# Kernel optimization log

Hardware: AMD Instinct MI355X
Metric: run time of the kernel (lower is better)

The kernel has to match this reference:

```python
import jax, jax.numpy as jnp
import numpy as np

L = 3          # GRU layers
H = 512        # hidden_dim == latent_dim == atom_vocab_size (required for source to run)
V = 512        # atom_vocab_size
B = 16
S = 96


def setup_inputs() -> dict:
    key = jax.random.key(0)
    ks = jax.random.split(key, 16)
    p = lambda k, shape: jax.random.normal(k, shape, dtype=jnp.float32) * 0.05
    return {
        "z": jax.random.normal(ks[0], (B, H), dtype=jnp.float32),
        "W_l2h": p(ks[1], (H, H)), "b_l2h": p(ks[2], (H,)),
        # GRU weights, torch gate order (r, z, n); stored [in, 3H] so x @ W
        "W_ih": p(ks[3], (L, H, 3 * H)), "W_hh": p(ks[4], (L, H, 3 * H)),
        "b_ih": p(ks[5], (L, 3 * H)), "b_hh": p(ks[6], (L, 3 * H)),
        # atom predictor MLP
        "Wa1": p(ks[7], (H, H)), "ba1": p(ks[8], (H,)),
        "Wa2": p(ks[9], (H, V)), "ba2": p(ks[10], (V,)),
        # bond predictor MLP (in = 2*V = 2*H)
        "Wb1": p(ks[11], (2 * H, H)), "bb1": p(ks[12], (H,)),
        "Wb2": p(ks[13], (H, 4)), "bb2": p(ks[14], (4,)),
        "target_length": S,
    }


def _gru_cell(hl, x, Wih_l, Whh_l, bih_l, bhh_l):
    gi = x @ Wih_l + bih_l          # [B, 3H]
    gh = hl @ Whh_l + bhh_l         # [B, 3H]
    ir, iz, inn = jnp.split(gi, 3, axis=-1)
    hr, hz, hn = jnp.split(gh, 3, axis=-1)
    r = jax.nn.sigmoid(ir + hr)
    zg = jax.nn.sigmoid(iz + hz)
    n = jnp.tanh(inn + r * hn)
    return (1.0 - zg) * n + zg * hl


def reference(z, W_l2h, b_l2h, W_ih, W_hh, b_ih, b_hh,
              Wa1, ba1, Wa2, ba2, Wb1, bb1, Wb2, bb2, target_length):
    batch = z.shape[0]
    seq_len = target_length
    h0 = z @ W_l2h + b_l2h                         # [B, H]
    hidden0 = jnp.broadcast_to(h0[None], (L, batch, H))  # repeat over layers

    x0 = jnp.zeros((batch, H), dtype=z.dtype)      # decoder input is zeros each step

    def step(hs, _):
        x = x0
        new = []
        for l in range(L):
            hl = _gru_cell(hs[l], x, W_ih[l], W_hh[l], b_ih[l], b_hh[l])
            new.append(hl)
            x = hl                                  # no inter-layer dropout (eval)
        logits = jax.nn.relu(x @ Wa1 + ba1) @ Wa2 + ba2   # [B, V]
        return jnp.stack(new), logits

    _, atoms = jax.lax.scan(step, hidden0, None, length=seq_len)  # [S, B, V]
    atoms = atoms.transpose(1, 0, 2)                # [B, S, V]
    atom_indices = jnp.argmax(atoms, axis=-1)       # argmax(softmax) == argmax(logits)

    # all-pairs bond MLP, vectorized: split first linear to avoid [B,S,S,2V] concat
    e_i = atoms @ Wb1[:V]                           # [B, S, H] (contribution of atom i)
    e_j = atoms @ Wb1[V:]                           # [B, S, H] (contribution of atom j)
    hp = jax.nn.relu(e_i[:, :, None, :] + e_j[:, None, :, :] + bb1)  # [B, S, S, H]
    edge = hp @ Wb2 + bb2                           # [B, S, S, 4]
    mask = 1.0 - jnp.eye(seq_len, dtype=edge.dtype)  # i == j entries stay zero
    edge = edge * mask[None, :, :, None]
    return atom_indices, edge
```

## Files before the change

### kernel.cpp

```cpp
#include <hip/hip_runtime.h>
#include <math.h>

#define H    512
#define TH3  1536
#define GRID 224

#define WS_STATE(l,p) ((size_t)((l)*3+(p)) * 8192)
#define WS_A1(p)      ((size_t)73728 + (size_t)(p)*8192)
#define WS_ATOMS      ((size_t)98304)
#define WS_E          ((size_t)884736)

__device__ __forceinline__ float sigm_(float x) { return 1.0f / (1.0f + expf(-x)); }

__device__ __forceinline__ float stampf(float x, unsigned b) {
    return __uint_as_float((__float_as_uint(x) & ~1u) | b);
}
__device__ __forceinline__ int lsb4ok(float4 v, unsigned e) {
    return ((__float_as_uint(v.x) & 1u) == e) & ((__float_as_uint(v.y) & 1u) == e) &
           ((__float_as_uint(v.z) & 1u) == e) & ((__float_as_uint(v.w) & 1u) == e);
}

__device__ __forceinline__ void ld_coh4(const float* p0, const float* p1,
                                        const float* p2, const float* p3,
                                        float4& a, float4& b, float4& c, float4& d)
{
    asm volatile(
        "global_load_dwordx4 %0, %4, off sc0 sc1\n\t"
        "global_load_dwordx4 %1, %5, off sc0 sc1\n\t"
        "global_load_dwordx4 %2, %6, off sc0 sc1\n\t"
        "global_load_dwordx4 %3, %7, off sc0 sc1\n\t"
        "s_waitcnt vmcnt(0)"
        : "=&v"(a), "=&v"(b), "=&v"(c), "=&v"(d)
        : "v"(p0), "v"(p1), "v"(p2), "v"(p3)
        : "memory");
}

__device__ __forceinline__ void ld_coh8(const float* p0, const float* p1,
                                        const float* p2, const float* p3,
                                        const float* p4, const float* p5,
                                        const float* p6, const float* p7,
                                        float4& a, float4& b, float4& c, float4& d,
                                        float4& e, float4& f, float4& g, float4& h)
{
    asm volatile(
        "global_load_dwordx4 %0, %8, off sc0 sc1\n\t"
        "global_load_dwordx4 %1, %9, off sc0 sc1\n\t"
        "global_load_dwordx4 %2, %10, off sc0 sc1\n\t"
        "global_load_dwordx4 %3, %11, off sc0 sc1\n\t"
        "global_load_dwordx4 %4, %12, off sc0 sc1\n\t"
        "global_load_dwordx4 %5, %13, off sc0 sc1\n\t"
        "global_load_dwordx4 %6, %14, off sc0 sc1\n\t"
        "global_load_dwordx4 %7, %15, off sc0 sc1\n\t"
        "s_waitcnt vmcnt(0)"
        : "=&v"(a), "=&v"(b), "=&v"(c), "=&v"(d),
          "=&v"(e), "=&v"(f), "=&v"(g), "=&v"(h)
        : "v"(p0), "v"(p1), "v"(p2), "v"(p3),
          "v"(p4), "v"(p5), "v"(p6), "v"(p7)
        : "memory");
}

__device__ __forceinline__ void st_coh1(float* p, float v) {
    asm volatile("global_store_dword %0, %1, off sc0 sc1" :: "v"(p), "v"(v) : "memory");
}

__device__ __forceinline__ void ld_coh_u32x2(const unsigned* p0, const unsigned* p1,
                                             unsigned& a, unsigned& b)
{
    asm volatile(
        "global_load_dword %0, %2, off sc0 sc1\n\t"
        "global_load_dword %1, %3, off sc0 sc1\n\t"
        "s_waitcnt vmcnt(0)"
        : "=&v"(a), "=&v"(b)
        : "v"(p0), "v"(p1)
        : "memory");
}

__device__ __forceinline__ void st_coh_u32(unsigned* p, unsigned v) {
    asm volatile("global_store_dword %0, %1, off sc0 sc1" :: "v"(p), "v"(v) : "memory");
}

template<int CTRL>
__device__ __forceinline__ float dppmov(float v) {
    return __int_as_float(__builtin_amdgcn_update_dpp(
        0, __float_as_int(v), CTRL, 0xF, 0xF, true));
}
#define DPP_XOR1 0xB1
#define DPP_XOR2 0x4E
#define DPP_XOR8 0x128

template<int PAT>
__device__ __forceinline__ float swzf(float v) {
    return __int_as_float(__builtin_amdgcn_ds_swizzle(__float_as_int(v), PAT));
}
#define SWZ_XOR4  0x101F
#define SWZ_XOR16 0x401F

extern "C" __global__ __launch_bounds__(256)
void k_init(const float* __restrict__ z, const float* __restrict__ Wl2h,
            const float* __restrict__ bl2h, float* __restrict__ ws)
{
    if (blockIdx.x == 0)
        ((unsigned*)(ws + WS_E))[threadIdx.x] = 0u;
    const int t  = threadIdx.x;
    const int jl = t & 15, b = t >> 4;
    const int j  = blockIdx.x * 16 + jl;
    float acc = 0.f;
    #pragma unroll 4
    for (int k = 0; k < H; ++k)
        acc += z[b * H + k] * Wl2h[(size_t)k * H + j];
    acc += bl2h[j];

    const int preh[3][3] = { { 1, 0, -1 },
                             { 0, -1, 1 },
                             { -1, 1, 0 } };
    #pragma unroll
    for (int l = 0; l < 3; ++l)
        #pragma unroll
        for (int p = 0; p < 3; ++p) {
            float v = (preh[l][p] < 0) ? stampf(acc, 1u)
                                       : __uint_as_float((unsigned)preh[l][p]);
            ws[WS_STATE(l, p) + j * 16 + b] = v;
        }
    const unsigned preA1[3] = { 1u, 0u, 0u };
    #pragma unroll
    for (int p = 0; p < 3; ++p)
        ws[WS_A1(p) + j * 16 + b] = __uint_as_float(preA1[p]);
}

__global__ __launch_bounds__(512, 2)
void k_gru(const float* __restrict__ W_ih, const float* __restrict__ W_hh,
           const float* __restrict__ b_ih, const float* __restrict__ b_hh,
           const float* __restrict__ Wa1,  const float* __restrict__ ba1,
           const float* __restrict__ Wa2,  const float* __restrict__ ba2,
           float* __restrict__ ws)
{
    __shared__ float sx[10240];
    __shared__ float sx2[10240];
    __shared__ float sh[10240];
    __shared__ float red[1536];
    unsigned* flags = (unsigned*)(ws + WS_E);

    const int bid = blockIdx.x;
    const int tid = threadIdx.x;

    int job, jbase;
    if      (bid < 64)  { job = 0; jbase = bid * 8; }
    else if (bid < 128) { job = 1; jbase = (bid - 64) * 8; }
    else if (bid < 192) { job = 2; jbase = (bid - 128) * 8; }
    else if (bid < 208) { job = 3; jbase = (bid - 192) * 32; }
    else                { job = 4; jbase = (bid - 208) * 32; }

    const int ks = tid & 31;
    const int cs = tid >> 6;

    int rs0, rc0;
    if      (job == 0) { rs0 = 0;   rc0 = 128; }
    else if (job == 1) { rs0 = 64;  rc0 = 128; }
    else if (job == 2) { rs0 = 128; rc0 = 80;  }
    else if (job == 3) { rs0 = 208; rc0 = 16;  }
    else               { rs0 = 0;   rc0 = 0;   }
    int fidl[2];
    #pragma unroll
    for (int e = 0; e < 2; ++e) {
        int idx = (tid & 63) + e * 64;
        fidl[e] = (idx < rc0) ? rs0 + idx : bid;
    }

    float w[6][16];
    if (job <= 2) {
        const int khalf = cs & 1, cpair = cs >> 1;
        const int colbase = jbase + cpair * 2;
        const float* WB = W_hh + (size_t)job * H * TH3;
        const float* WA = W_ih + (size_t)job * H * TH3;
        #pragma unroll
        for (int f = 0; f < 6; ++f) {
            int g = f >> 1, c = f & 1;
            #pragma unroll
            for (int kk = 0; kk < 8; ++kk) {
                size_t ro = (size_t)(khalf * 256 + kk * 32 + ks) * TH3 + g * 512 + colbase + c;
                w[f][8 + kk] = WB[ro];
                if (job != 0) w[f][kk] = WA[ro];
            }
        }
    } else {
        const float* base = (job == 3) ? Wa1 : Wa2;
        const int colbase = jbase + cs * 4;
        #pragma unroll
        for (int f = 0; f < 4; ++f)
            #pragma unroll
            for (int kk = 0; kk < 16; ++kk)
                w[f][kk] = base[(size_t)(kk * 32 + ks) * H + colbase + f];
    }

    float c_bi0 = 0, c_bi1 = 0, c_bi2 = 0, c_bh0 = 0, c_bh1 = 0, c_bh2 = 0;
    float hp = 0.f, c_ba = 0.f;
    if (job <= 2) {
        if (tid < 128) {
            int b = tid & 15, j2 = tid >> 4, jc = jbase + j2;
            const float* bi  = b_ih + (size_t)job * TH3;
            const float* bhh = b_hh + (size_t)job * TH3;
            c_bi0 = bi[jc]; c_bi1 = bi[512 + jc]; c_bi2 = bi[1024 + jc];
            c_bh0 = bhh[jc]; c_bh1 = bhh[512 + jc]; c_bh2 = bhh[1024 + jc];
            const int hpp = (job == 0) ? 2 : (job == 1) ? 1 : 0;
            hp = ws[WS_STATE(job, hpp) + jc * 16 + b];
        }
    } else if (job == 3) {
        c_ba = ba1[jbase + (tid >> 4)];
    } else {
        c_ba = ba2[jbase + (tid & 31)];
    }

    auto stage32k = [&](const float* src, unsigned eb, float* dst) {
        const int k0 = tid >> 2, q4 = (tid & 3) * 4;
        float4 a, b, c, d;
        for (;;) {
            ld_coh4(src + 4 * tid, src + 4 * (tid + 512),
                    src + 4 * (tid + 1024), src + 4 * (tid + 1536), a, b, c, d);
            if (__all(lsb4ok(a, eb) & lsb4ok(b, eb) & lsb4ok(c, eb) & lsb4ok(d, eb)))
                break;
            __builtin_amdgcn_s_sleep(1);
        }
        *(float4*)&dst[(k0      ) * 20 + q4] = a;
        *(float4*)&dst[(k0 + 128) * 20 + q4] = b;
        *(float4*)&dst[(k0 + 256) * 20 + q4] = c;
        *(float4*)&dst[(k0 + 384) * 20 + q4] = d;
    };

    auto stage64k = [&](const float* srcH, const float* srcX, unsigned eb,
                        float* dstH, float* dstX) {
        const int k0 = tid >> 2, q4 = (tid & 3) * 4;
        float4 xa, xb, xc, xd, ha, hb, hc, hd;
        for (;;) {
            ld_coh8(srcX + 4 * tid, srcX + 4 * (tid + 512),
                    srcX + 4 * (tid + 1024), srcX + 4 * (tid + 1536),
                    srcH + 4 * tid, srcH + 4 * (tid + 512),
                    srcH + 4 * (tid + 1024), srcH + 4 * (tid + 1536),
                    xa, xb, xc, xd, ha, hb, hc, hd);
            int ok = lsb4ok(xa, eb) & lsb4ok(xb, eb) & lsb4ok(xc, eb) & lsb4ok(xd, eb) &
                     lsb4ok(ha, eb) & lsb4ok(hb, eb) & lsb4ok(hc, eb) & lsb4ok(hd, eb);
            if (__all(ok)) break;
            __builtin_amdgcn_s_sleep(1);
        }
        *(float4*)&dstX[(k0      ) * 20 + q4] = xa;
        *(float4*)&dstX[(k0 + 128) * 20 + q4] = xb;
        *(float4*)&dstX[(k0 + 256) * 20 + q4] = xc;
        *(float4*)&dstX[(k0 + 384) * 20 + q4] = xd;
        *(float4*)&dstH[(k0      ) * 20 + q4] = ha;
        *(float4*)&dstH[(k0 + 128) * 20 + q4] = hb;
        *(float4*)&dstH[(k0 + 256) * 20 + q4] = hc;
        *(float4*)&dstH[(k0 + 384) * 20 + q4] = hd;
    };

    auto mv6 = [&](const float* arr, int wo, int redbase) {
        const int qh = (tid >> 5) & 1;
        const int rowoff = 8 * qh;
        const bool b0 = (ks & 1), b1 = (ks & 2), b3 = (ks & 8), b4 = (ks & 16);
        const float* base = arr + (cs & 1) * (256 * 20);
        float acc[6][8];
        #pragma unroll
        for (int f = 0; f < 6; ++f)
            #pragma unroll
            for (int i = 0; i < 8; ++i) acc[f][i] = 0.f;
        #pragma unroll
        for (int kk = 0; kk < 8; ++kk) {
            const float* p = base + (kk * 32 + ks) * 20 + rowoff;
            float4 v0 = *(const float4*)p;
            float4 v1 = *(const float4*)(p + 4);
            #pragma unroll
            for (int f = 0; f < 6; ++f) {
                float wv = w[f][wo + kk];
                acc[f][0] += wv * v0.x; acc[f][1] += wv * v0.y;
                acc[f][2] += wv * v0.z; acc[f][3] += wv * v0.w;
                acc[f][4] += wv * v1.x; acc[f][5] += wv * v1.y;
                acc[f][6] += wv * v1.z; acc[f][7] += wv * v1.w;
            }
        }
        float a[6];
        #pragma unroll
        for (int f = 0; f < 6; ++f) {
            float t[4];
            #pragma unroll
            for (int j = 0; j < 4; ++j) {
                float give = b0 ? acc[f][j] : acc[f][j + 4];
                float recv = dppmov<DPP_XOR1>(give);
                float keep = b0 ? acc[f][j + 4] : acc[f][j];
                t[j] = keep + recv;
            }
            float u[2];
            #pragma unroll
            for (int j = 0; j < 2; ++j) {
                float give = b1 ? t[j] : t[j + 2];
                float recv = dppmov<DPP_XOR2>(give);
                float keep = b1 ? t[j + 2] : t[j];
                u[j] = keep + recv;
            }
            float give = b3 ? u[0] : u[1];
            float recv = dppmov<DPP_XOR8>(give);
            float keep = b3 ? u[1] : u[0];
            a[f] = keep + recv;
        }
        #pragma unroll
        for (int f = 0; f < 6; ++f) a[f] += swzf<SWZ_XOR4>(a[f]);
        float r[3];
        #pragma unroll
        for (int i = 0; i < 3; ++i) {
            float give = b4 ? a[i] : a[i + 3];
            float recv = swzf<SWZ_XOR16>(give);
            float keep = b4 ? a[i + 3] : a[i];
            r[i] = keep + recv;
        }
        if (!(ks & 4)) {
            int bl = ((ks & 1) << 2) | (ks & 2) | ((ks >> 3) & 1);
            int bb = ((tid >> 5) & 1) * 8 + bl;
            int fb3 = ((ks >> 4) & 1) * 3;
            #pragma unroll
            for (int i = 0; i < 3; ++i) {
                int f = fb3 + i, g = f >> 1, c = f & 1;
                red[redbase + (cs & 1) * 384 + g * 128 + ((cs >> 1) * 2 + c) * 16 + bb] = r[i];
            }
        }
    };

    auto mv4 = [&](const float* arr) {
        const int qh = (tid >> 5) & 1;
        const int rowoff = 8 * qh;
        const bool b0 = (ks & 1), b1 = (ks & 2), b3 = (ks & 8), b4 = (ks & 16);
        float acc[4][8];
        #pragma unroll
        for (int f = 0; f < 4; ++f)
            #pragma unroll
            for (int i = 0; i < 8; ++i) acc[f][i] = 0.f;
        #pragma unroll
        for (int kk = 0; kk < 16; ++kk) {
            const float* p = arr + (kk * 32 + ks) * 20 + rowoff;
            float4 v0 = *(const float4*)p;
            float4 v1 = *(const float4*)(p + 4);
            #pragma unroll
            for (int f = 0; f < 4; ++f) {
                float wv = w[f][kk];
                acc[f][0] += wv * v0.x; acc[f][1] += wv * v0.y;
                acc[f][2] += wv * v0.z; acc[f][3] += wv * v0.w;
                acc[f][4] += wv * v1.x; acc[f][5] += wv * v1.y;
                acc[f][6] += wv * v1.z; acc[f][7] += wv * v1.w;
            }
        }
        float a[4];
        #pragma unroll
        for (int f = 0; f < 4; ++f) {
            float t[4];
            #pragma unroll
            for (int j = 0; j < 4; ++j) {
                float give = b0 ? acc[f][j] : acc[f][j + 4];
                float recv = dppmov<DPP_XOR1>(give);
                float keep = b0 ? acc[f][j + 4] : acc[f][j];
                t[j] = keep + recv;
            }
            float u[2];
            #pragma unroll
            for (int j = 0; j < 2; ++j) {
                float give = b1 ? t[j] : t[j + 2];
                float recv = dppmov<DPP_XOR2>(give);
                float keep = b1 ? t[j + 2] : t[j];
                u[j] = keep + recv;
            }
            float give = b3 ? u[0] : u[1];
            float recv = dppmov<DPP_XOR8>(give);
            float keep = b3 ? u[1] : u[0];
            a[f] = keep + recv;
        }
        #pragma unroll
        for (int f = 0; f < 4; ++f) a[f] += swzf<SWZ_XOR4>(a[f]);
        float r[2];
        #pragma unroll
        for (int i = 0; i < 2; ++i) {
            float give = b4 ? a[i] : a[i + 2];
            float recv = swzf<SWZ_XOR16>(give);
            float keep = b4 ? a[i + 2] : a[i];
            r[i] = keep + recv;
        }
        if (!(ks & 4)) {
            int bl = ((ks & 1) << 2) | (ks & 2) | ((ks >> 3) & 1);
            int bb = ((tid >> 5) & 1) * 8 + bl;
            int f2 = ((ks >> 4) & 1) * 2;
            #pragma unroll
            for (int i = 0; i < 2; ++i)
                red[(cs * 4 + f2 + i) * 16 + bb] = r[i];
        }
    };

    for (int s = 0; s < 102; ++s) {
        const int rp = (s + 2) % 3, wp = s % 3;
        const unsigned expb = (unsigned)((s + 1) & 1);
        const unsigned myb  = (unsigned)(s & 1);
        int act;
        if      (job == 0) act = (s <= 95);
        else if (job == 1) act = (s >= 2 && s <= 97);
        else if (job == 2) act = (s >= 4 && s <= 99);
        else if (job == 3) act = (s >= 5 && s <= 100);
        else               act = (s >= 6 && s <= 101);
        const int s0 = (job == 1) ? 2 : 4;
        const int dox = (job == 1 || job == 2) && (s >= s0 - 1) && (s <= s0 + 94);
        float* rbuf = (s & 1) ? sx2 : sx;
        float* wbuf = (s & 1) ? sx : sx2;

        if (act) {
            if (tid < 64 && s >= 2) {
                unsigned lim = (unsigned)(s - 1);
                for (;;) {
                    unsigned v0, v1;
                    ld_coh_u32x2(&flags[fidl[0]], &flags[fidl[1]], v0, v1);
                    if (__all((int)((v0 >= lim) & (v1 >= lim)))) break;
                    __builtin_amdgcn_s_sleep(1);
                }
            }

            if (job == 1 || job == 2) {
                mv6(rbuf, 0, 0);
                if (dox)
                    stage64k(ws + WS_STATE(job, rp), ws + WS_STATE(job - 1, rp),
                             expb, sh, wbuf);
                else
                    stage32k(ws + WS_STATE(job, rp), expb, sh);
                __syncthreads();
                mv6(sh, 8, 768);
                __syncthreads();
                if (tid < 128) {
                    int b = tid & 15, jc = jbase + (tid >> 4);
                    int o = tid;
                    float gi0 = red[o]        + red[384 + o];
                    float gi1 = red[128 + o]  + red[512 + o];
                    float gi2 = red[256 + o]  + red[640 + o];
                    float gh0 = red[768 + o]  + red[1152 + o];
                    float gh1 = red[896 + o]  + red[1280 + o];
                    float gh2 = red[1024 + o] + red[1408 + o];
                    float r  = sigm_(gi0 + c_bi0 + gh0 + c_bh0);
                    float zg = sigm_(gi1 + c_bi1 + gh1 + c_bh1);
                    float n  = tanhf(gi2 + c_bi2 + r * (gh2 + c_bh2));
                    float hn = (1.f - zg) * n + zg * hp;
                    hp = hn;
                    st_coh1(&ws[WS_STATE(job, wp) + jc * 16 + b], stampf(hn, myb));
                }
            } else if (job == 0) {
                stage32k(ws + WS_STATE(0, rp), expb, sx);
                __syncthreads();
                mv6(sx, 8, 768);
                __syncthreads();
                if (tid < 128) {
                    int b = tid & 15, jc = jbase + (tid >> 4);
                    int o = tid;
                    float g0 = red[768 + o]  + red[1152 + o];
                    float g1 = red[896 + o]  + red[1280 + o];
                    float g2 = red[1024 + o] + red[1408 + o];
                    float r  = sigm_(c_bi0 + g0 + c_bh0);
                    float zg = sigm_(c_bi1 + g1 + c_bh1);
                    float n  = tanhf(c_bi2 + r * (g2 + c_bh2));
                    float hn = (1.f - zg) * n + zg * hp;
                    hp = hn;
                    st_coh1(&ws[WS_STATE(0, wp) + jc * 16 + b], stampf(hn, myb));
                }
            } else {
                const float* srcp = (job == 3) ? (ws + WS_STATE(2, rp))
                                               : (ws + WS_A1(rp));
                stage32k(srcp, expb, sx);
                __syncthreads();
                mv4(sx);
                __syncthreads();
                if (job == 3) {
                    int b = tid & 15, j2 = tid >> 4, jc = jbase + j2;
                    float v = red[j2 * 16 + b] + c_ba;
                    st_coh1(&ws[WS_A1(wp) + jc * 16 + b], stampf(fmaxf(v, 0.f), myb));
                } else {
                    int j2 = tid & 31, b = tid >> 5, jc = jbase + j2;
                    float v = red[j2 * 16 + b] + c_ba;
                    ws[WS_ATOMS + ((size_t)(s - 6) * 16 + b) * H + jc] = v;
                }
            }
        } else if (dox) {
            stage32k(ws + WS_STATE(job - 1, rp), expb, wbuf);
        }

        __syncthreads();
        if (tid == 0) st_coh_u32(&flags[bid], (unsigned)(s + 1));
    }
}

extern "C" __global__ __launch_bounds__(256)
void k_argmax(const float* __restrict__ ws, float* __restrict__ out)
{
    const int t = blockIdx.x;
    const int wv = threadIdx.x >> 6, lane = threadIdx.x & 63;
    for (int b = wv; b < 16; b += 4) {
        const float* row = ws + WS_ATOMS + ((size_t)t * 16 + b) * H;
        float mx = -3.4028235e38f; int mi = 0;
        #pragma unroll
        for (int c = 0; c < 8; ++c) {
            int idx = lane + c * 64;
            float v = row[idx];
            if (v > mx) { mx = v; mi = idx; }
        }
        #pragma unroll
        for (int off = 32; off >= 1; off >>= 1) {
            float omx = __shfl_down(mx, off);
            int   omi = __shfl_down(mi, off);
            if (omx > mx || (omx == mx && omi < mi)) { mx = omx; mi = omi; }
        }
        if (lane == 0) out[b * 96 + t] = (float)mi;
    }
}

extern "C" __global__ __launch_bounds__(256)
void k_eij(const float* __restrict__ Wb1, const float* __restrict__ bb1,
           float* __restrict__ ws)
{
    __shared__ float aT[8192];
    const int bid = blockIdx.x;
    const int t = bid >> 4, m = (bid >> 3) & 1, ct = bid & 7;
    const int tid = threadIdx.x;
    const float* atoms = ws + WS_ATOMS;
    for (int f = tid; f < 2048; f += 256) {
        int b = f >> 7, kq = f & 127;
        float4 v = ((const float4*)(atoms + ((size_t)(t * 16 + b)) * H))[kq];
        aT[(kq * 4 + 0) * 16 + b] = v.x;
        aT[(kq * 4 + 1) * 16 + b] = v.y;
        aT[(kq * 4 + 2) * 16 + b] = v.z;
        aT[(kq * 4 + 3) * 16 + b] = v.w;
    }
    __syncthreads();
    const int c = tid & 63, rq = tid >> 6;
    const int col = ct * 64 + c;
    const float* Wp = Wb1 + (size_t)m * H * H + col;
    float a0 = 0, a1 = 0, a2 = 0, a3 = 0;
    #pragma unroll 8
    for (int k = 0; k < 512; ++k) {
        float  wv = Wp[(size_t)k * H];
        float4 av = *(const float4*)&aT[k * 16 + rq * 4];
        a0 += av.x * wv; a1 += av.y * wv; a2 += av.z * wv; a3 += av.w * wv;
    }
    float bb = (m == 0) ? bb1[col] : 0.f;
    a0 += bb; a1 += bb; a2 += bb; a3 += bb;
    float* eb = ws + WS_E + (size_t)(m * 16) * 96 * H;
    eb[((size_t)(rq * 4 + 0) * 96 + t) * H + col] = a0;
    eb[((size_t)(rq * 4 + 1) * 96 + t) * H + col] = a1;
    eb[((size_t)(rq * 4 + 2) * 96 + t) * H + col] = a2;
    eb[((size_t)(rq * 4 + 3) * 96 + t) * H + col] = a3;
}

extern "C" __global__ __launch_bounds__(256)
void k_edge(const float* __restrict__ Wb2, const float* __restrict__ bb2,
            const float* __restrict__ ws, float* __restrict__ out)
{
    __shared__ float ls[32][260];
    __shared__ float wsm[2048];
    const int bid = blockIdx.x;
    const int b = bid / 36, r6 = bid % 36, it = r6 / 6, jt = r6 % 6;
    const int tid = threadIdx.x;
    const int ip = tid & 15, jp = tid >> 4;
    float acc0 = 0, acc1 = 0, acc2 = 0, acc3 = 0;

    for (int f = tid; f < 2048; f += 256)
        wsm[f] = Wb2[f];

    for (int ph = 0; ph < 2; ++ph) {
        __syncthreads();
        for (int f = tid; f < 2048; f += 256) {
            int r = f >> 6, c4 = f & 63;
            const float* src = (r < 16)
                ? ws + WS_E + ((size_t)b * 96 + it * 16 + r) * H
                : ws + WS_E + ((size_t)(16 + b) * 96 + jt * 16 + (r - 16)) * H;
            float4 v = *(const float4*)(src + ph * 256 + c4 * 4);
            *(float4*)&ls[r][c4 * 4] = v;
        }
        __syncthreads();
        const float* wb = &wsm[ph * 1024];
        #pragma unroll 2
        for (int hh = 0; hh < 256; hh += 4) {
            float4 ei = *(const float4*)&ls[ip][hh];
            float4 ej = *(const float4*)&ls[16 + jp][hh];
            float4 w0 = *(const float4*)(wb + (size_t)hh * 4);
            float4 w1 = *(const float4*)(wb + (size_t)hh * 4 + 4);
            float4 w2 = *(const float4*)(wb + (size_t)hh * 4 + 8);
            float4 w3 = *(const float4*)(wb + (size_t)hh * 4 + 12);
            float v;
            v = fmaxf(ei.x + ej.x, 0.f); acc0 += v * w0.x; acc1 += v * w0.y; acc2 += v * w0.z; acc3 += v * w0.w;
            v = fmaxf(ei.y + ej.y, 0.f); acc0 += v * w1.x; acc1 += v * w1.y; acc2 += v * w1.z; acc3 += v * w1.w;
            v = fmaxf(ei.z + ej.z, 0.f); acc0 += v * w2.x; acc1 += v * w2.y; acc2 += v * w2.z; acc3 += v * w2.w;
            v = fmaxf(ei.w + ej.w, 0.f); acc0 += v * w3.x; acc1 += v * w3.y; acc2 += v * w3.z; acc3 += v * w3.w;
        }
    }
    const int i = it * 16 + ip, j = jt * 16 + jp;
    float4 o;
    if (i == j) { o.x = 0.f; o.y = 0.f; o.z = 0.f; o.w = 0.f; }
    else { o.x = acc0 + bb2[0]; o.y = acc1 + bb2[1]; o.z = acc2 + bb2[2]; o.w = acc3 + bb2[3]; }
    *(float4*)(out + 1536 + (((size_t)b * 96 + i) * 96 + j) * 4) = o;
}

extern "C" void kernel_launch(void* const* d_in, const int* in_sizes, int n_in,
                              void* d_out, int out_size, void* d_ws, size_t ws_size,
                              hipStream_t stream)
{
    const float* z    = (const float*)d_in[0];
    const float* Wl2h = (const float*)d_in[1];
    const float* bl2h = (const float*)d_in[2];
    const float* W_ih = (const float*)d_in[3];
    const float* W_hh = (const float*)d_in[4];
    const float* b_ih = (const float*)d_in[5];
    const float* b_hh = (const float*)d_in[6];
    const float* Wa1  = (const float*)d_in[7];
    const float* ba1  = (const float*)d_in[8];
    const float* Wa2  = (const float*)d_in[9];
    const float* ba2  = (const float*)d_in[10];
    const float* Wb1  = (const float*)d_in[11];
    const float* bb1  = (const float*)d_in[12];
    const float* Wb2  = (const float*)d_in[13];
    const float* bb2  = (const float*)d_in[14];
    float* out = (float*)d_out;
    float* ws  = (float*)d_ws;

    hipLaunchKernelGGL(k_init, dim3(32), dim3(256), 0, stream, z, Wl2h, bl2h, ws);

    hipLaunchKernelGGL(k_gru, dim3(GRID), dim3(512), 0, stream,
                       W_ih, W_hh, b_ih, b_hh, Wa1, ba1, Wa2, ba2, ws);

    hipLaunchKernelGGL(k_argmax, dim3(96), dim3(256), 0, stream, ws, out);
    hipLaunchKernelGGL(k_eij, dim3(1536), dim3(256), 0, stream, Wb1, bb1, ws);
    hipLaunchKernelGGL(k_edge, dim3(576), dim3(256), 0, stream, Wb2, bb2, ws, out);
}
```

Measured before the change: 798.8 us.

## Post step flags early and prefetch GRU state loads before flag wait

Each block now publishes its step-completion flag right after staging its input into shared memory instead of at the end of the step, so producer blocks can overwrite the triple-buffered state sooner. For layers 1 and 2, the coherent loads of the input and hidden state are issued before the flag spin and the first matvec, and are waited on afterwards, hiding load latency behind compute. This relies on the triple buffering and LSB stamp checks to stay correct once flags are released early, and the prefetched values may be stale, which forces a reload loop.

```diff
diff --git a/kernel.cpp b/kernel.cpp
--- a/kernel.cpp
+++ b/kernel.cpp
@@ -59,6 +59,34 @@
         : "memory");
 }
 
+__device__ __forceinline__ void ld_coh8_issue(const float* p0, const float* p1,
+                                              const float* p2, const float* p3,
+                                              const float* p4, const float* p5,
+                                              const float* p6, const float* p7,
+                                              float4& a, float4& b, float4& c, float4& d,
+                                              float4& e, float4& f, float4& g, float4& h)
+{
+    asm volatile(
+        "global_load_dwordx4 %0, %8, off sc0 sc1\n\t"
+        "global_load_dwordx4 %1, %9, off sc0 sc1\n\t"
+        "global_load_dwordx4 %2, %10, off sc0 sc1\n\t"
+        "global_load_dwordx4 %3, %11, off sc0 sc1\n\t"
+        "global_load_dwordx4 %4, %12, off sc0 sc1\n\t"
+        "global_load_dwordx4 %5, %13, off sc0 sc1\n\t"
+        "global_load_dwordx4 %6, %14, off sc0 sc1\n\t"
+        "global_load_dwordx4 %7, %15, off sc0 sc1"
+        : "=&v"(a), "=&v"(b), "=&v"(c), "=&v"(d),
+          "=&v"(e), "=&v"(f), "=&v"(g), "=&v"(h)
+        : "v"(p0), "v"(p1), "v"(p2), "v"(p3),
+          "v"(p4), "v"(p5), "v"(p6), "v"(p7)
+        : "memory");
+}
+
+__device__ __forceinline__ void vm_wait0() {
+    asm volatile("s_waitcnt vmcnt(0)" ::: "memory");
+    __builtin_amdgcn_sched_barrier(0);
+}
+
 __device__ __forceinline__ void st_coh1(float* p, float v) {
     asm volatile("global_store_dword %0, %1, off sc0 sc1" :: "v"(p), "v"(v) : "memory");
 }
@@ -224,31 +252,6 @@
         *(float4*)&dst[(k0 + 128) * 20 + q4] = b;
         *(float4*)&dst[(k0 + 256) * 20 + q4] = c;
         *(float4*)&dst[(k0 + 384) * 20 + q4] = d;
-    };
-
-    auto stage64k = [&](const float* srcH, const float* srcX, unsigned eb,
-                        float* dstH, float* dstX) {
-        const int k0 = tid >> 2, q4 = (tid & 3) * 4;
-        float4 xa, xb, xc, xd, ha, hb, hc, hd;
-        for (;;) {
-            ld_coh8(srcX + 4 * tid, srcX + 4 * (tid + 512),
-                    srcX + 4 * (tid + 1024), srcX + 4 * (tid + 1536),
-                    srcH + 4 * tid, srcH + 4 * (tid + 512),
-                    srcH + 4 * (tid + 1024), srcH + 4 * (tid + 1536),
-                    xa, xb, xc, xd, ha, hb, hc, hd);
-            int ok = lsb4ok(xa, eb) & lsb4ok(xb, eb) & lsb4ok(xc, eb) & lsb4ok(xd, eb) &
-                     lsb4ok(ha, eb) & lsb4ok(hb, eb) & lsb4ok(hc, eb) & lsb4ok(hd, eb);
-            if (__all(ok)) break;
-            __builtin_amdgcn_s_sleep(1);
-        }
-        *(float4*)&dstX[(k0      ) * 20 + q4] = xa;
-        *(float4*)&dstX[(k0 + 128) * 20 + q4] = xb;
-        *(float4*)&dstX[(k0 + 256) * 20 + q4] = xc;
-        *(float4*)&dstX[(k0 + 384) * 20 + q4] = xd;
-        *(float4*)&dstH[(k0      ) * 20 + q4] = ha;
-        *(float4*)&dstH[(k0 + 128) * 20 + q4] = hb;
-        *(float4*)&dstH[(k0 + 256) * 20 + q4] = hc;
-        *(float4*)&dstH[(k0 + 384) * 20 + q4] = hd;
     };
 
     auto mv6 = [&](const float* arr, int wo, int redbase) {
@@ -402,26 +405,65 @@
         const int dox = (job == 1 || job == 2) && (s >= s0 - 1) && (s <= s0 + 94);
         float* rbuf = (s & 1) ? sx2 : sx;
         float* wbuf = (s & 1) ? sx : sx2;
+        bool posted = false;
 
         if (act) {
-            if (tid < 64 && s >= 2) {
-                unsigned lim = (unsigned)(s - 1);
-                for (;;) {
-                    unsigned v0, v1;
-                    ld_coh_u32x2(&flags[fidl[0]], &flags[fidl[1]], v0, v1);
-                    if (__all((int)((v0 >= lim) & (v1 >= lim)))) break;
-                    __builtin_amdgcn_s_sleep(1);
+            if (job == 1 || job == 2) {
+                const float* srcH = ws + WS_STATE(job, rp);
+                const float* srcX = ws + WS_STATE(job - 1, rp);
+                const int k0 = tid >> 2, q4 = (tid & 3) * 4;
+                float4 xa, xb, xc, xd, ha, hb, hc, hd;
+                if (dox)
+                    ld_coh8_issue(srcX + 4 * tid, srcX + 4 * (tid + 512),
+                                  srcX + 4 * (tid + 1024), srcX + 4 * (tid + 1536),
+                                  srcH + 4 * tid, srcH + 4 * (tid + 512),
+                                  srcH + 4 * (tid + 1024), srcH + 4 * (tid + 1536),
+                                  xa, xb, xc, xd, ha, hb, hc, hd);
+
+                if (tid < 64 && s >= 2) {
+                    unsigned lim = (unsigned)(s - 1);
+                    for (;;) {
+                        unsigned v0, v1;
+                        ld_coh_u32x2(&flags[fidl[0]], &flags[fidl[1]], v0, v1);
+                        if (__all((int)((v0 >= lim) & (v1 >= lim)))) break;
+                        __builtin_amdgcn_s_sleep(1);
+                    }
                 }
-            }
-
-            if (job == 1 || job == 2) {
+
                 mv6(rbuf, 0, 0);
-                if (dox)
-                    stage64k(ws + WS_STATE(job, rp), ws + WS_STATE(job - 1, rp),
-                             expb, sh, wbuf);
-                else
-                    stage32k(ws + WS_STATE(job, rp), expb, sh);
+
+                if (dox) {
+                    vm_wait0();
+                    int ok = lsb4ok(xa, expb) & lsb4ok(xb, expb) &
+                             lsb4ok(xc, expb) & lsb4ok(xd, expb) &
+                             lsb4ok(ha, expb) & lsb4ok(hb, expb) &
+                             lsb4ok(hc, expb) & lsb4ok(hd, expb);
+                    while (!__all(ok)) {
+                        __builtin_amdgcn_s_sleep(1);
+                        ld_coh8(srcX + 4 * tid, srcX + 4 * (tid + 512),
+                                srcX + 4 * (tid + 1024), srcX + 4 * (tid + 1536),
+                                srcH + 4 * tid, srcH + 4 * (tid + 512),
+                                srcH + 4 * (tid + 1024), srcH + 4 * (tid + 1536),
+                                xa, xb, xc, xd, ha, hb, hc, hd);
+                        ok = lsb4ok(xa, expb) & lsb4ok(xb, expb) &
+                             lsb4ok(xc, expb) & lsb4ok(xd, expb) &
+                             lsb4ok(ha, expb) & lsb4ok(hb, expb) &
+                             lsb4ok(hc, expb) & lsb4ok(hd, expb);
+                    }
+                    *(float4*)&wbuf[(k0      ) * 20 + q4] = xa;
+                    *(float4*)&wbuf[(k0 + 128) * 20 + q4] = xb;
+                    *(float4*)&wbuf[(k0 + 256) * 20 + q4] = xc;
+                    *(float4*)&wbuf[(k0 + 384) * 20 + q4] = xd;
+                    *(float4*)&sh[(k0      ) * 20 + q4] = ha;
+                    *(float4*)&sh[(k0 + 128) * 20 + q4] = hb;
+                    *(float4*)&sh[(k0 + 256) * 20 + q4] = hc;
+                    *(float4*)&sh[(k0 + 384) * 20 + q4] = hd;
+                } else {
+                    stage32k(srcH, expb, sh);
+                }
                 __syncthreads();
+                if (tid == 0) st_coh_u32(&flags[bid], (unsigned)(s + 1));
+                posted = true;
                 mv6(sh, 8, 768);
                 __syncthreads();
                 if (tid < 128) {
@@ -441,8 +483,19 @@
                     st_coh1(&ws[WS_STATE(job, wp) + jc * 16 + b], stampf(hn, myb));
                 }
             } else if (job == 0) {
+                if (tid < 64 && s >= 2) {
+                    unsigned lim = (unsigned)(s - 1);
+                    for (;;) {
+                        unsigned v0, v1;
+                        ld_coh_u32x2(&flags[fidl[0]], &flags[fidl[1]], v0, v1);
+                        if (__all((int)((v0 >= lim) & (v1 >= lim)))) break;
+                        __builtin_amdgcn_s_sleep(1);
+                    }
+                }
                 stage32k(ws + WS_STATE(0, rp), expb, sx);
                 __syncthreads();
+                if (tid == 0) st_coh_u32(&flags[bid], (unsigned)(s + 1));
+                posted = true;
                 mv6(sx, 8, 768);
                 __syncthreads();
                 if (tid < 128) {
@@ -459,10 +512,21 @@
                     st_coh1(&ws[WS_STATE(0, wp) + jc * 16 + b], stampf(hn, myb));
                 }
             } else {
+                if (tid < 64 && s >= 2) {
+                    unsigned lim = (unsigned)(s - 1);
+                    for (;;) {
+                        unsigned v0, v1;
+                        ld_coh_u32x2(&flags[fidl[0]], &flags[fidl[1]], v0, v1);
+                        if (__all((int)((v0 >= lim) & (v1 >= lim)))) break;
+                        __builtin_amdgcn_s_sleep(1);
+                    }
+                }
                 const float* srcp = (job == 3) ? (ws + WS_STATE(2, rp))
                                                : (ws + WS_A1(rp));
                 stage32k(srcp, expb, sx);
                 __syncthreads();
+                if (tid == 0) st_coh_u32(&flags[bid], (unsigned)(s + 1));
+                posted = true;
                 mv4(sx);
                 __syncthreads();
                 if (job == 3) {
@@ -480,7 +544,7 @@
         }
 
         __syncthreads();
-        if (tid == 0) st_coh_u32(&flags[bid], (unsigned)(s + 1));
+        if (!posted && tid == 0) st_coh_u32(&flags[bid], (unsigned)(s + 1));
     }
 }
 
```

Result: no change. 807.9 us (+1.1%).

## Overlap flag polling with staging and post step flag right after staging

Applied to the files above, without the earlier changes.

The readiness-flag loads are now issued before staging the state buffers and checked only after staging, which hides the flag-load latency. Each block also posts its completion flag right after the staged data has been consumed into LDS, not at the end of the step. This lets downstream and upstream blocks in the persistent pipeline proceed sooner. The risk lies in the protocol: staging reads data before the flag is confirmed, so correctness rests on the LSB stamp checks and the triple buffering to prevent overwrites. An early post could let producers overwrite a buffer that is still being read.

```diff
diff --git a/kernel.cpp b/kernel.cpp
--- a/kernel.cpp
+++ b/kernel.cpp
@@ -59,6 +59,11 @@
         : "memory");
 }
 
+__device__ __forceinline__ void vm_wait0() {
+    asm volatile("s_waitcnt vmcnt(0)" ::: "memory");
+    __builtin_amdgcn_sched_barrier(0);
+}
+
 __device__ __forceinline__ void st_coh1(float* p, float v) {
     asm volatile("global_store_dword %0, %1, off sc0 sc1" :: "v"(p), "v"(v) : "memory");
 }
@@ -70,6 +75,17 @@
         "global_load_dword %0, %2, off sc0 sc1\n\t"
         "global_load_dword %1, %3, off sc0 sc1\n\t"
         "s_waitcnt vmcnt(0)"
+        : "=&v"(a), "=&v"(b)
+        : "v"(p0), "v"(p1)
+        : "memory");
+}
+
+__device__ __forceinline__ void ld_coh_u32x2_issue(const unsigned* p0, const unsigned* p1,
+                                                   unsigned& a, unsigned& b)
+{
+    asm volatile(
+        "global_load_dword %0, %2, off sc0 sc1\n\t"
+        "global_load_dword %1, %3, off sc0 sc1"
         : "=&v"(a), "=&v"(b)
         : "v"(p0), "v"(p1)
         : "memory");
@@ -251,6 +267,17 @@
         *(float4*)&dstH[(k0 + 384) * 20 + q4] = hd;
     };
 
+    auto flagchk = [&](unsigned fv0, unsigned fv1, unsigned lim) {
+        if (!__all((int)((fv0 >= lim) & (fv1 >= lim)))) {
+            for (;;) {
+                __builtin_amdgcn_s_sleep(1);
+                unsigned v0, v1;
+                ld_coh_u32x2(&flags[fidl[0]], &flags[fidl[1]], v0, v1);
+                if (__all((int)((v0 >= lim) & (v1 >= lim)))) break;
+            }
+        }
+    };
+
     auto mv6 = [&](const float* arr, int wo, int redbase) {
         const int qh = (tid >> 5) & 1;
         const int rowoff = 8 * qh;
@@ -402,26 +429,26 @@
         const int dox = (job == 1 || job == 2) && (s >= s0 - 1) && (s <= s0 + 94);
         float* rbuf = (s & 1) ? sx2 : sx;
         float* wbuf = (s & 1) ? sx : sx2;
+        bool posted = false;
 
         if (act) {
-            if (tid < 64 && s >= 2) {
-                unsigned lim = (unsigned)(s - 1);
-                for (;;) {
-                    unsigned v0, v1;
-                    ld_coh_u32x2(&flags[fidl[0]], &flags[fidl[1]], v0, v1);
-                    if (__all((int)((v0 >= lim) & (v1 >= lim)))) break;
-                    __builtin_amdgcn_s_sleep(1);
-                }
-            }
+            unsigned fv0 = 0xFFFFFFFFu, fv1 = 0xFFFFFFFFu;
+            const bool needchk = (tid < 64) && (s >= 2);
+            if (needchk)
+                ld_coh_u32x2_issue(&flags[fidl[0]], &flags[fidl[1]], fv0, fv1);
 
             if (job == 1 || job == 2) {
+                const float* srcH = ws + WS_STATE(job, rp);
+                const float* srcX = ws + WS_STATE(job - 1, rp);
                 mv6(rbuf, 0, 0);
                 if (dox)
-                    stage64k(ws + WS_STATE(job, rp), ws + WS_STATE(job - 1, rp),
-                             expb, sh, wbuf);
+                    stage64k(srcH, srcX, expb, sh, wbuf);
                 else
-                    stage32k(ws + WS_STATE(job, rp), expb, sh);
+                    stage32k(srcH, expb, sh);
+                if (needchk) { vm_wait0(); flagchk(fv0, fv1, (unsigned)(s - 1)); }
                 __syncthreads();
+                if (tid == 0) st_coh_u32(&flags[bid], (unsigned)(s + 1));
+                posted = true;
                 mv6(sh, 8, 768);
                 __syncthreads();
                 if (tid < 128) {
@@ -442,7 +469,10 @@
                 }
             } else if (job == 0) {
                 stage32k(ws + WS_STATE(0, rp), expb, sx);
+                if (needchk) { vm_wait0(); flagchk(fv0, fv1, (unsigned)(s - 1)); }
                 __syncthreads();
+                if (tid == 0) st_coh_u32(&flags[bid], (unsigned)(s + 1));
+                posted = true;
                 mv6(sx, 8, 768);
                 __syncthreads();
                 if (tid < 128) {
@@ -462,7 +492,10 @@
                 const float* srcp = (job == 3) ? (ws + WS_STATE(2, rp))
                                                : (ws + WS_A1(rp));
                 stage32k(srcp, expb, sx);
+                if (needchk) { vm_wait0(); flagchk(fv0, fv1, (unsigned)(s - 1)); }
                 __syncthreads();
+                if (tid == 0) st_coh_u32(&flags[bid], (unsigned)(s + 1));
+                posted = true;
                 mv4(sx);
                 __syncthreads();
                 if (job == 3) {
@@ -480,7 +513,7 @@
         }
 
         __syncthreads();
-        if (tid == 0) st_coh_u32(&flags[bid], (unsigned)(s + 1));
+        if (!posted && tid == 0) st_coh_u32(&flags[bid], (unsigned)(s + 1));
     }
 }
 
```

Result: faster. 734.6 us (-8.0%).
